# Performance work log

Hardware: AMD Instinct MI355X
Metric: run time of the kernel (lower is better)

The kernel has to match this reference:

```python
import jax, jax.numpy as jnp
import numpy as np

B, F, H, E, O = 512, 512, 512, 8, 512  # batch, feature, hidden, experts, out_frame


def setup_inputs() -> dict:
    key = jax.random.key(0)
    ks = jax.random.split(key, 14)
    u = lambda k, shape, s: jax.random.uniform(k, shape, jnp.float32) * s
    return {
        "x": jax.random.normal(ks[0], (B, F), jnp.float32),
        # gating MLP params (torch Linear: y = x @ W.T + b)
        "gw0": u(ks[1], (H, F), 0.04) - 0.02,
        "gb0": jnp.zeros((H,), jnp.float32),
        "gw1": u(ks[2], (H, H), 0.04) - 0.02,
        "gb1": jnp.zeros((H,), jnp.float32),
        "gw2": u(ks[3], (E, H), 0.04) - 0.02,
        "gb2": jnp.zeros((E,), jnp.float32),
        # expert weight/bias banks
        "alpha0": u(ks[4], (E, H, F), 0.01),
        "beta0": jnp.zeros((E, H, 1), jnp.float32),
        "alpha1": u(ks[5], (E, H, H), 0.01),
        "beta1": jnp.zeros((E, H, 1), jnp.float32),
        "alpha2": u(ks[6], (E, O, H), 0.01),
        "beta2": jnp.zeros((E, O, 1), jnp.float32),
    }


def reference(x, gw0, gb0, gw1, gb1, gw2, gb2,
              alpha0, beta0, alpha1, beta1, alpha2, beta2):
    # gating network
    h = jax.nn.elu(x @ gw0.T + gb0)
    h = jax.nn.elu(h @ gw1.T + gb1)
    g = jax.nn.softmax(h @ gw2.T + gb2, axis=1)  # [B, E]

    # per-sample blended weights (sum over experts of gate-scaled expert mats)
    blend_w = lambda a: jnp.einsum('be,ehf->bhf', g, a)
    blend_b = lambda b: jnp.einsum('be,eh->bh', g, b[..., 0])

    # per-sample 3-layer MLP (bmm with vector rhs == batched matvec)
    H1 = jax.nn.elu(jnp.einsum('bhf,bf->bh', blend_w(alpha0), x) + blend_b(beta0))
    H2 = jax.nn.elu(jnp.einsum('bhf,bf->bh', blend_w(alpha1), H1) + blend_b(beta1))
    H3 = jnp.einsum('bof,bf->bo', blend_w(alpha2), H2) + blend_b(beta2)
    return H3
```

## Files before the change

### kernel.cpp

```cpp
#include <hip/hip_runtime.h>
#include <hip/hip_bf16.h>
#include <math.h>

enum { Bq = 512, Fq = 512, Hq = 512, Eq = 8, Oq = 512 };

typedef __attribute__((ext_vector_type(8))) short short8;
typedef __attribute__((ext_vector_type(4))) float floatx4;

static __device__ __forceinline__ unsigned short f2bf(float f) {
  unsigned u = __float_as_uint(f);
  u += 0x7fffu + ((u >> 16) & 1u);
  return (unsigned short)(u >> 16);
}
static __device__ __forceinline__ float bf2f(unsigned short h) {
  return __uint_as_float(((unsigned)h) << 16);
}
static __device__ __forceinline__ float elu1(float v) {
  return v > 0.f ? v : (__expf(v) - 1.f);
}

typedef __attribute__((address_space(1))) const unsigned int gu32;
typedef __attribute__((address_space(3))) unsigned int lu32;
static __device__ __forceinline__ void gld16(const unsigned short* g,
                                             unsigned short* l) {
  __builtin_amdgcn_global_load_lds((gu32*)g, (lu32*)l, 16, 0, 0);
}

__global__ __launch_bounds__(256) void cvt6_kernel(
    const float* __restrict__ b0, const float* __restrict__ b1,
    const float* __restrict__ b2, unsigned short* __restrict__ db0,
    unsigned short* __restrict__ db1, unsigned short* __restrict__ db2,
    const float* __restrict__ s0, const float* __restrict__ s1,
    const float* __restrict__ s2, unsigned short* __restrict__ ds0,
    unsigned short* __restrict__ ds1, unsigned short* __restrict__ ds2,
    int nb, int ns) {
  int i = blockIdx.x * 256 + threadIdx.x;
  const float4* s;
  unsigned short* d;
  int j;
  if (i < 3 * nb) {
    int seg = i / nb;
    j = i - seg * nb;
    s = (seg == 0) ? (const float4*)b0
      : (seg == 1) ? (const float4*)b1 : (const float4*)b2;
    d = (seg == 0) ? db0 : (seg == 1) ? db1 : db2;
  } else {
    int k = i - 3 * nb;
    if (k >= 3 * ns) return;
    int seg = k / ns;
    j = k - seg * ns;
    s = (seg == 0) ? (const float4*)s0
      : (seg == 1) ? (const float4*)s1 : (const float4*)s2;
    d = (seg == 0) ? ds0 : (seg == 1) ? ds1 : ds2;
  }
  float4 v = s[j];
  ushort4 o;
  o.x = f2bf(v.x); o.y = f2bf(v.y); o.z = f2bf(v.z); o.w = f2bf(v.w);
  *(ushort4*)(d + 4 * (size_t)j) = o;
}

template <int BM, int BN, int BK, int TM, int TN, int EPI, int KS>
__global__ __launch_bounds__(256) void gemm_bt(
    const unsigned short* __restrict__ A, const unsigned short* __restrict__ W,
    const float* __restrict__ bias, float* __restrict__ Cf,
    unsigned short* __restrict__ Cb, int M, int N, int K) {
  __shared__ unsigned short As[BM * BK];
  __shared__ unsigned short Bs[BN * BK];
  const int tid = threadIdx.x;
  const int wave = tid >> 6, lane = tid & 63;
  const int wm = wave >> 1, wn = wave & 1;
  const int lr = lane & 15, lk = lane >> 4;
  const int m0 = blockIdx.y * BM, n0 = blockIdx.x * BN;
  const int Ksl = K / KS;
  const int kbeg = blockIdx.z * Ksl, kend = kbeg + Ksl;
  constexpr int WMt = BM / 2, WNt = BN / 2;
  constexpr int CPR = BK / 8;
  constexpr int CHA = BM * CPR, CHB = BN * CPR;

  floatx4 acc[TM][TN];
#pragma unroll
  for (int i = 0; i < TM; i++)
#pragma unroll
    for (int j = 0; j < TN; j++) acc[i][j] = (floatx4){0.f, 0.f, 0.f, 0.f};

  for (int k0 = kbeg; k0 < kend; k0 += BK) {
#pragma unroll
    for (int c = tid; c < CHA; c += 256) {
      int r = c / CPR, q = c % CPR;
      gld16(&A[(size_t)(m0 + r) * K + k0 + q * 8], &As[(c & ~63) * 8]);
    }
#pragma unroll
    for (int c = tid; c < CHB; c += 256) {
      int r = c / CPR, q = c % CPR;
      gld16(&W[(size_t)(n0 + r) * K + k0 + q * 8], &Bs[(c & ~63) * 8]);
    }
    __syncthreads();
#pragma unroll
    for (int kk = 0; kk < BK; kk += 32) {
      short8 af[TM], bw[TN];
#pragma unroll
      for (int i = 0; i < TM; i++)
        af[i] = *(const short8*)&As[(wm * WMt + i * 16 + lr) * BK + kk + lk * 8];
#pragma unroll
      for (int j = 0; j < TN; j++)
        bw[j] = *(const short8*)&Bs[(wn * WNt + j * 16 + lr) * BK + kk + lk * 8];
#pragma unroll
      for (int i = 0; i < TM; i++)
#pragma unroll
        for (int j = 0; j < TN; j++)
          acc[i][j] = __builtin_amdgcn_mfma_f32_16x16x32_bf16(
              af[i], bw[j], acc[i][j], 0, 0, 0);
    }
    __syncthreads();
  }

  float* Cfo = Cf + (size_t)blockIdx.z * M * N;
#pragma unroll
  for (int i = 0; i < TM; i++) {
#pragma unroll
    for (int j = 0; j < TN; j++) {
#pragma unroll
      for (int r = 0; r < 4; r++) {
        int m = m0 + wm * WMt + i * 16 + lk * 4 + r;
        int n = n0 + wn * WNt + j * 16 + lr;
        float v = acc[i][j][r];
        if (EPI == 0) {
          Cfo[(size_t)m * N + n] = v;
        } else {
          v += bias[n];
          Cb[(size_t)m * N + n] = f2bf(elu1(v));
        }
      }
    }
  }
}

__global__ __launch_bounds__(64) void gate_kernel(
    const unsigned short* __restrict__ G1,
    const float* __restrict__ gw2,
    const float* __restrict__ gb2,
    float* __restrict__ g) {
  int b = blockIdx.x;
  int lane = threadIdx.x;
  float xv[8];
#pragma unroll
  for (int t = 0; t < 8; t++) xv[t] = bf2f(G1[(size_t)b * Hq + t * 64 + lane]);
  float le[Eq];
#pragma unroll
  for (int e = 0; e < Eq; e++) {
    float p = 0.f;
#pragma unroll
    for (int t = 0; t < 8; t++)
      p += xv[t] * gw2[(size_t)e * Hq + t * 64 + lane];
#pragma unroll
    for (int o = 32; o > 0; o >>= 1) p += __shfl_xor(p, o);
    le[e] = p + gb2[e];
  }
  float m = le[0];
#pragma unroll
  for (int e = 1; e < Eq; e++) m = fmaxf(m, le[e]);
  float s = 0.f;
#pragma unroll
  for (int e = 0; e < Eq; e++) {
    le[e] = __expf(le[e] - m);
    s += le[e];
  }
  float inv = 1.f / s;
  if (lane == 0) {
#pragma unroll
    for (int e = 0; e < Eq; e++) g[(size_t)b * Eq + e] = le[e] * inv;
  }
}

template <int ACT, int KS>
__global__ __launch_bounds__(256) void combine_kernel(
    const float* __restrict__ Y,
    const float* __restrict__ g,
    const float* __restrict__ beta,
    unsigned short* __restrict__ outb, float* __restrict__ outf) {
  int idx = blockIdx.x * 256 + threadIdx.x;
  int b = idx >> 9, h = idx & 511;
  const float* gb = g + (size_t)b * Eq;
  const float* y = Y + (size_t)b * Eq * Hq;
  float s = 0.f;
#pragma unroll
  for (int e = 0; e < Eq; e++) {
    float ye = beta[e * Hq + h];
#pragma unroll
    for (int p = 0; p < KS; p++)
      ye += y[(size_t)p * Bq * Eq * Hq + e * Hq + h];
    s += gb[e] * ye;
  }
  if (ACT)
    outb[idx] = f2bf(elu1(s));
  else
    outf[idx] = s;
}

extern "C" void kernel_launch(void* const* d_in, const int* in_sizes, int n_in,
                              void* d_out, int out_size, void* d_ws,
                              size_t ws_size, hipStream_t stream) {
  const float* x = (const float*)d_in[0];
  const float* gw0 = (const float*)d_in[1];
  const float* gb0 = (const float*)d_in[2];
  const float* gw1 = (const float*)d_in[3];
  const float* gb1 = (const float*)d_in[4];
  const float* gw2 = (const float*)d_in[5];
  const float* gb2 = (const float*)d_in[6];
  const float* alpha0 = (const float*)d_in[7];
  const float* beta0 = (const float*)d_in[8];
  const float* alpha1 = (const float*)d_in[9];
  const float* beta1 = (const float*)d_in[10];
  const float* alpha2 = (const float*)d_in[11];
  const float* beta2 = (const float*)d_in[12];
  float* out = (float*)d_out;

  char* ws = (char*)d_ws;
  auto alloc = [&](size_t bytes) {
    char* p = ws;
    ws += (bytes + 255) & ~(size_t)255;
    return p;
  };
  unsigned short* xb = (unsigned short*)alloc((size_t)Bq * Fq * 2);
  unsigned short* gw0b = (unsigned short*)alloc((size_t)Hq * Fq * 2);
  unsigned short* gw1b = (unsigned short*)alloc((size_t)Hq * Hq * 2);
  unsigned short* a0b = (unsigned short*)alloc((size_t)Eq * Hq * Fq * 2);
  unsigned short* a1b = (unsigned short*)alloc((size_t)Eq * Hq * Hq * 2);
  unsigned short* a2b = (unsigned short*)alloc((size_t)Eq * Oq * Hq * 2);
  unsigned short* G0b = (unsigned short*)alloc((size_t)Bq * Hq * 2);
  unsigned short* G1b = (unsigned short*)alloc((size_t)Bq * Hq * 2);
  unsigned short* H1b = (unsigned short*)alloc((size_t)Bq * Hq * 2);
  unsigned short* H2b = (unsigned short*)alloc((size_t)Bq * Hq * 2);
  float* gates = (float*)alloc((size_t)Bq * Eq * 4);
  float* Y = (float*)alloc((size_t)2 * Bq * Eq * Hq * 4);

  {
    int nb = (Eq * Hq * Fq) / 4, ns = (Bq * Fq) / 4;
    int total = 3 * nb + 3 * ns;
    cvt6_kernel<<<(total + 255) / 256, 256, 0, stream>>>(
        alpha0, alpha1, alpha2, a0b, a1b, a2b, x, gw0, gw1, xb, gw0b, gw1b,
        nb, ns);
  }

  dim3 gg(Hq / 64, Bq / 32);
  gemm_bt<32, 64, 64, 1, 2, 1, 1><<<gg, 256, 0, stream>>>(
      xb, gw0b, gb0, nullptr, G0b, Bq, Hq, Fq);
  gemm_bt<32, 64, 64, 1, 2, 1, 1><<<gg, 256, 0, stream>>>(
      G0b, gw1b, gb1, nullptr, G1b, Bq, Hq, Hq);

  gate_kernel<<<Bq, 64, 0, stream>>>(G1b, gw2, gb2, gates);

  dim3 ge((Eq * Hq) / 128, Bq / 128, 2);
  gemm_bt<128, 128, 64, 4, 4, 0, 2><<<ge, 256, 0, stream>>>(
      xb, a0b, nullptr, Y, nullptr, Bq, Eq * Hq, Fq);
  combine_kernel<1, 2><<<(Bq * Hq) / 256, 256, 0, stream>>>(Y, gates, beta0,
                                                            H1b, nullptr);
  gemm_bt<128, 128, 64, 4, 4, 0, 2><<<ge, 256, 0, stream>>>(
      H1b, a1b, nullptr, Y, nullptr, Bq, Eq * Hq, Hq);
  combine_kernel<1, 2><<<(Bq * Hq) / 256, 256, 0, stream>>>(Y, gates, beta1,
                                                            H2b, nullptr);
  gemm_bt<128, 128, 64, 4, 4, 0, 2><<<ge, 256, 0, stream>>>(
      H2b, a2b, nullptr, Y, nullptr, Bq, Eq * Oq, Hq);
  combine_kernel<0, 2><<<(Bq * Oq) / 256, 256, 0, stream>>>(Y, gates, beta2,
                                                            nullptr, out);
}
```

Measured before the change: 162.3 us.

## Split expert GEMMs per expert with gate-scaled epilogue and vectorized partial reduction

Replaces the wide expert GEMM over all experts with a per-expert, split-K grid whose epilogue multiplies each partial by the sample's gate value. A new reduce kernel sums the 16 partial slices with float4 loads, adds the gated bias, and applies ELU. This raises block count for better CU occupancy and removes per-element gate multiplies in the reduce step, at the cost of smaller tiles and the same large fp32 intermediate traffic.

```diff
diff --git a/kernel.cpp b/kernel.cpp
--- a/kernel.cpp
+++ b/kernel.cpp
@@ -59,11 +59,11 @@
   *(ushort4*)(d + 4 * (size_t)j) = o;
 }
 
-template <int BM, int BN, int BK, int TM, int TN, int EPI, int KS>
+template <int BM, int BN, int BK, int TM, int TN>
 __global__ __launch_bounds__(256) void gemm_bt(
     const unsigned short* __restrict__ A, const unsigned short* __restrict__ W,
-    const float* __restrict__ bias, float* __restrict__ Cf,
-    unsigned short* __restrict__ Cb, int M, int N, int K) {
+    const float* __restrict__ bias, unsigned short* __restrict__ Cb,
+    int M, int N, int K) {
   __shared__ unsigned short As[BM * BK];
   __shared__ unsigned short Bs[BN * BK];
   const int tid = threadIdx.x;
@@ -71,8 +71,6 @@
   const int wm = wave >> 1, wn = wave & 1;
   const int lr = lane & 15, lk = lane >> 4;
   const int m0 = blockIdx.y * BM, n0 = blockIdx.x * BN;
-  const int Ksl = K / KS;
-  const int kbeg = blockIdx.z * Ksl, kend = kbeg + Ksl;
   constexpr int WMt = BM / 2, WNt = BN / 2;
   constexpr int CPR = BK / 8;
   constexpr int CHA = BM * CPR, CHB = BN * CPR;
@@ -83,7 +81,7 @@
 #pragma unroll
     for (int j = 0; j < TN; j++) acc[i][j] = (floatx4){0.f, 0.f, 0.f, 0.f};
 
-  for (int k0 = kbeg; k0 < kend; k0 += BK) {
+  for (int k0 = 0; k0 < K; k0 += BK) {
 #pragma unroll
     for (int c = tid; c < CHA; c += 256) {
       int r = c / CPR, q = c % CPR;
@@ -114,7 +112,6 @@
     __syncthreads();
   }
 
-  float* Cfo = Cf + (size_t)blockIdx.z * M * N;
 #pragma unroll
   for (int i = 0; i < TM; i++) {
 #pragma unroll
@@ -123,13 +120,80 @@
       for (int r = 0; r < 4; r++) {
         int m = m0 + wm * WMt + i * 16 + lk * 4 + r;
         int n = n0 + wn * WNt + j * 16 + lr;
-        float v = acc[i][j][r];
-        if (EPI == 0) {
-          Cfo[(size_t)m * N + n] = v;
-        } else {
-          v += bias[n];
-          Cb[(size_t)m * N + n] = f2bf(elu1(v));
-        }
+        float v = acc[i][j][r] + bias[n];
+        Cb[(size_t)m * N + n] = f2bf(elu1(v));
+      }
+    }
+  }
+}
+
+template <int BM, int BN, int BK, int TM, int TN>
+__global__ __launch_bounds__(256) void expert_gemm(
+    const unsigned short* __restrict__ A,
+    const unsigned short* __restrict__ Wb,
+    const float* __restrict__ g,
+    float* __restrict__ P) {
+  __shared__ unsigned short As[BM * BK];
+  __shared__ unsigned short Bs[BN * BK];
+  const int tid = threadIdx.x;
+  const int wave = tid >> 6, lane = tid & 63;
+  const int wm = wave >> 1, wn = wave & 1;
+  const int lr = lane & 15, lk = lane >> 4;
+  const int m0 = blockIdx.y * BM, n0 = blockIdx.x * BN;
+  const int e = blockIdx.z >> 1, ks = blockIdx.z & 1;
+  const int kbeg = ks * 256, kend = kbeg + 256;
+  const unsigned short* W = Wb + (size_t)e * Hq * 512 + (size_t)n0 * 512;
+  constexpr int WMt = BM / 2, WNt = BN / 2;
+  constexpr int CPR = BK / 8;
+  constexpr int CHA = BM * CPR, CHB = BN * CPR;
+
+  floatx4 acc[TM][TN];
+#pragma unroll
+  for (int i = 0; i < TM; i++)
+#pragma unroll
+    for (int j = 0; j < TN; j++) acc[i][j] = (floatx4){0.f, 0.f, 0.f, 0.f};
+
+  for (int k0 = kbeg; k0 < kend; k0 += BK) {
+#pragma unroll
+    for (int c = tid; c < CHA; c += 256) {
+      int r = c / CPR, q = c % CPR;
+      gld16(&A[(size_t)(m0 + r) * 512 + k0 + q * 8], &As[(c & ~63) * 8]);
+    }
+#pragma unroll
+    for (int c = tid; c < CHB; c += 256) {
+      int r = c / CPR, q = c % CPR;
+      gld16(&W[(size_t)r * 512 + k0 + q * 8], &Bs[(c & ~63) * 8]);
+    }
+    __syncthreads();
+#pragma unroll
+    for (int kk = 0; kk < BK; kk += 32) {
+      short8 af[TM], bw[TN];
+#pragma unroll
+      for (int i = 0; i < TM; i++)
+        af[i] = *(const short8*)&As[(wm * WMt + i * 16 + lr) * BK + kk + lk * 8];
+#pragma unroll
+      for (int j = 0; j < TN; j++)
+        bw[j] = *(const short8*)&Bs[(wn * WNt + j * 16 + lr) * BK + kk + lk * 8];
+#pragma unroll
+      for (int i = 0; i < TM; i++)
+#pragma unroll
+        for (int j = 0; j < TN; j++)
+          acc[i][j] = __builtin_amdgcn_mfma_f32_16x16x32_bf16(
+              af[i], bw[j], acc[i][j], 0, 0, 0);
+    }
+    __syncthreads();
+  }
+
+  float* Po = P + (size_t)blockIdx.z * Bq * Hq;
+#pragma unroll
+  for (int i = 0; i < TM; i++) {
+#pragma unroll
+    for (int j = 0; j < TN; j++) {
+#pragma unroll
+      for (int r = 0; r < 4; r++) {
+        int m = m0 + wm * WMt + i * 16 + lk * 4 + r;
+        int n = n0 + wn * WNt + j * 16 + lr;
+        Po[(size_t)m * Hq + n] = acc[i][j][r] * g[m * Eq + e];
       }
     }
   }
@@ -172,29 +236,35 @@
   }
 }
 
-template <int ACT, int KS>
-__global__ __launch_bounds__(256) void combine_kernel(
-    const float* __restrict__ Y,
+template <int ACT>
+__global__ __launch_bounds__(256) void reduce_kernel(
+    const float* __restrict__ P,
     const float* __restrict__ g,
     const float* __restrict__ beta,
     unsigned short* __restrict__ outb, float* __restrict__ outf) {
   int idx = blockIdx.x * 256 + threadIdx.x;
-  int b = idx >> 9, h = idx & 511;
+  int b = idx >> 7, h4 = (idx & 127) << 2;
+  float4 s = {0.f, 0.f, 0.f, 0.f};
+#pragma unroll
+  for (int z = 0; z < 16; z++) {
+    float4 v = *(const float4*)&P[((size_t)z * Bq + b) * Hq + h4];
+    s.x += v.x; s.y += v.y; s.z += v.z; s.w += v.w;
+  }
   const float* gb = g + (size_t)b * Eq;
-  const float* y = Y + (size_t)b * Eq * Hq;
-  float s = 0.f;
 #pragma unroll
   for (int e = 0; e < Eq; e++) {
-    float ye = beta[e * Hq + h];
-#pragma unroll
-    for (int p = 0; p < KS; p++)
-      ye += y[(size_t)p * Bq * Eq * Hq + e * Hq + h];
-    s += gb[e] * ye;
-  }
-  if (ACT)
-    outb[idx] = f2bf(elu1(s));
-  else
-    outf[idx] = s;
+    float ge = gb[e];
+    float4 bv = *(const float4*)&beta[e * Hq + h4];
+    s.x += ge * bv.x; s.y += ge * bv.y; s.z += ge * bv.z; s.w += ge * bv.w;
+  }
+  if (ACT) {
+    ushort4 o;
+    o.x = f2bf(elu1(s.x)); o.y = f2bf(elu1(s.y));
+    o.z = f2bf(elu1(s.z)); o.w = f2bf(elu1(s.w));
+    *(ushort4*)&outb[(size_t)idx * 4] = o;
+  } else {
+    *(float4*)&outf[(size_t)idx * 4] = s;
+  }
 }
 
 extern "C" void kernel_launch(void* const* d_in, const int* in_sizes, int n_in,
@@ -232,7 +302,7 @@
   unsigned short* H1b = (unsigned short*)alloc((size_t)Bq * Hq * 2);
   unsigned short* H2b = (unsigned short*)alloc((size_t)Bq * Hq * 2);
   float* gates = (float*)alloc((size_t)Bq * Eq * 4);
-  float* Y = (float*)alloc((size_t)2 * Bq * Eq * Hq * 4);
+  float* P = (float*)alloc((size_t)16 * Bq * Hq * 4);
 
   {
     int nb = (Eq * Hq * Fq) / 4, ns = (Bq * Fq) / 4;
@@ -243,24 +313,19 @@
   }
 
   dim3 gg(Hq / 64, Bq / 32);
-  gemm_bt<32, 64, 64, 1, 2, 1, 1><<<gg, 256, 0, stream>>>(
-      xb, gw0b, gb0, nullptr, G0b, Bq, Hq, Fq);
-  gemm_bt<32, 64, 64, 1, 2, 1, 1><<<gg, 256, 0, stream>>>(
-      G0b, gw1b, gb1, nullptr, G1b, Bq, Hq, Hq);
+  gemm_bt<32, 64, 64, 1, 2><<<gg, 256, 0, stream>>>(xb, gw0b, gb0, G0b,
+                                                    Bq, Hq, Fq);
+  gemm_bt<32, 64, 64, 1, 2><<<gg, 256, 0, stream>>>(G0b, gw1b, gb1, G1b,
+                                                    Bq, Hq, Hq);
 
   gate_kernel<<<Bq, 64, 0, stream>>>(G1b, gw2, gb2, gates);
 
-  dim3 ge((Eq * Hq) / 128, Bq / 128, 2);
-  gemm_bt<128, 128, 64, 4, 4, 0, 2><<<ge, 256, 0, stream>>>(
-      xb, a0b, nullptr, Y, nullptr, Bq, Eq * Hq, Fq);
-  combine_kernel<1, 2><<<(Bq * Hq) / 256, 256, 0, stream>>>(Y, gates, beta0,
-                                                            H1b, nullptr);
-  gemm_bt<128, 128, 64, 4, 4, 0, 2><<<ge, 256, 0, stream>>>(
-      H1b, a1b, nullptr, Y, nullptr, Bq, Eq * Hq, Hq);
-  combine_kernel<1, 2><<<(Bq * Hq) / 256, 256, 0, stream>>>(Y, gates, beta1,
-                                                            H2b, nullptr);
-  gemm_bt<128, 128, 64, 4, 4, 0, 2><<<ge, 256, 0, stream>>>(
-      H2b, a2b, nullptr, Y, nullptr, Bq, Eq * Oq, Hq);
-  combine_kernel<0, 2><<<(Bq * Oq) / 256, 256, 0, stream>>>(Y, gates, beta2,
-                                                            nullptr, out);
-}
+  dim3 ge(Hq / 128, Bq / 64, Eq * 2);
+  dim3 gr((Bq * Hq / 4) / 256);
+  expert_gemm<64, 128, 64, 2, 4><<<ge, 256, 0, stream>>>(xb, a0b, gates, P);
+  reduce_kernel<1><<<gr, 256, 0, stream>>>(P, gates, beta0, H1b, nullptr);
+  expert_gemm<64, 128, 64, 2, 4><<<ge, 256, 0, stream>>>(H1b, a1b, gates, P);
+  reduce_kernel<1><<<gr, 256, 0, stream>>>(P, gates, beta1, H2b, nullptr);
+  expert_gemm<64, 128, 64, 2, 4><<<ge, 256, 0, stream>>>(H2b, a2b, gates, P);
+  reduce_kernel<0><<<gr, 256, 0, stream>>>(P, gates, beta2, nullptr, out);
+}
```

Measured after the change: 164.2 us. About the same (+1.2%).
